# Optimization experiments

Measured on AMD Instinct MI355X. Metric: run time of the kernel, lower is better.

Reference implementation:

```python
import jax, jax.numpy as jnp
import numpy as np

DIM = 2048
N_HEADS = 16
N_KV_HEADS = 4
HEAD_DIM = DIM // N_HEADS  # 128
N_REP = N_HEADS // N_KV_HEADS
EPS = 1e-6


def rmsnorm(x, w):
    norm = jax.lax.rsqrt(jnp.mean(x * x, axis=-1, keepdims=True) + EPS)
    return x * norm * w


def apply_rope(xq, xk, freqs_cis):
    # xq: (B,S,Hq,D), xk: (B,S,Hk,D); freqs_cis: (S, D/2, 2) -> (cos, sin)
    cos = freqs_cis[None, :, None, :, 0]  # (1,S,1,D/2)
    sin = freqs_cis[None, :, None, :, 1]

    def rot(x):
        xr = x.reshape(*x.shape[:-1], HEAD_DIM // 2, 2)
        x0, x1 = xr[..., 0], xr[..., 1]
        o0 = x0 * cos - x1 * sin
        o1 = x0 * sin + x1 * cos
        return jnp.stack([o0, o1], axis=-1).reshape(x.shape)

    return rot(xq), rot(xk)


def setup_inputs() -> dict:
    key = jax.random.key(0)
    k1, k2, k3, k4, k5, k6 = jax.random.split(key, 6)
    B, S = 2, 2048
    x = jax.random.normal(k1, (B, S, DIM), dtype=jnp.float32)
    x_mask = jnp.ones((B, S), dtype=bool)
    freqs_cis = jax.random.uniform(k2, (S, HEAD_DIM // 2, 2), dtype=jnp.float32)
    qkv_out = (N_HEADS + 2 * N_KV_HEADS) * HEAD_DIM  # 3072
    w_qkv = jax.random.normal(k3, (qkv_out, DIM), dtype=jnp.float32) * (DIM ** -0.5)
    w_out = jax.random.normal(k4, (DIM, N_HEADS * HEAD_DIM), dtype=jnp.float32) * (DIM ** -0.5)
    qn_w = jnp.ones((HEAD_DIM,), dtype=jnp.float32)
    kn_w = jnp.ones((HEAD_DIM,), dtype=jnp.float32)
    return {"x": x, "x_mask": x_mask, "freqs_cis": freqs_cis,
            "w_qkv": w_qkv, "w_out": w_out, "qn_w": qn_w, "kn_w": kn_w}


def reference(x, x_mask, freqs_cis, w_qkv, w_out, qn_w, kn_w):
    B, S, _ = x.shape
    qkv = x @ w_qkv.T  # (B,S,3072)
    dq = N_HEADS * HEAD_DIM
    dkv = N_KV_HEADS * HEAD_DIM
    xq = qkv[..., :dq].reshape(B, S, N_HEADS, HEAD_DIM)
    xk = qkv[..., dq:dq + dkv].reshape(B, S, N_KV_HEADS, HEAD_DIM)
    xv = qkv[..., dq + dkv:].reshape(B, S, N_KV_HEADS, HEAD_DIM)
    xq = rmsnorm(xq, qn_w)
    xk = rmsnorm(xk, kn_w)
    xq, xk = apply_rope(xq, xk, freqs_cis)
    # GQA: repeat kv heads
    xk = jnp.repeat(xk, N_REP, axis=2)  # (B,S,H,D)
    xv = jnp.repeat(xv, N_REP, axis=2)
    # SDPA: (B,H,S,D)
    q = jnp.moveaxis(xq, 1, 2)
    k = jnp.moveaxis(xk, 1, 2)
    v = jnp.moveaxis(xv, 1, 2)
    scale = HEAD_DIM ** -0.5
    scores = jnp.einsum('bhqd,bhkd->bhqk', q, k) * scale
    bias = jnp.where(x_mask[:, None, None, :], 0.0, -jnp.inf).astype(q.dtype)
    attn = jax.nn.softmax(scores + bias, axis=-1)
    out = jnp.einsum('bhqk,bhkd->bhqd', attn, v)
    out = jnp.moveaxis(out, 1, 2).reshape(B, S, N_HEADS * HEAD_DIM)
    return out @ w_out.T
```

## Files before the change

kernel.cpp:

```cpp
#include <hip/hip_runtime.h>
#include <hip/hip_bf16.h>

#define DIMSZ 2048
#define SLEN  2048
#define NH    16
#define NKV   4
#define HD    128
#define NTOK  4096
#define QKVN  3072

typedef __bf16 bf16x8 __attribute__((ext_vector_type(8)));
typedef __bf16 bf16x4 __attribute__((ext_vector_type(4)));
typedef short  s16x4  __attribute__((ext_vector_type(4)));
typedef float  floatx4 __attribute__((ext_vector_type(4)));

__device__ __forceinline__ void async16(const __bf16* g, __bf16* l) {
    __builtin_amdgcn_global_load_lds(
        (const __attribute__((address_space(1))) void*)g,
        (__attribute__((address_space(3))) void*)l, 16, 0, 0);
}

__device__ __forceinline__ floatx4 mfma16x16x16_bf16(s16x4 a, s16x4 b, floatx4 c) {
#if __has_builtin(__builtin_amdgcn_mfma_f32_16x16x16bf16_1k)
    return __builtin_amdgcn_mfma_f32_16x16x16bf16_1k(a, b, c, 0, 0, 0);
#else
    asm volatile("v_mfma_f32_16x16x16_bf16 %0, %1, %2, %0"
                 : "+v"(c) : "v"(a), "v"(b));
    return c;
#endif
}

__global__ __launch_bounds__(256) void cvt3(const float* __restrict__ s0, __bf16* __restrict__ d0, int n0,
                                            const float* __restrict__ s1, __bf16* __restrict__ d1, int n1,
                                            const float* __restrict__ s2, __bf16* __restrict__ d2, int n2) {
    int blk = blockIdx.x;
    int b0 = n0 >> 11, b1 = n1 >> 11;
    const float* s; __bf16* d; int base;
    if (blk < b0)           { s = s0; d = d0; base = blk << 11; }
    else if (blk < b0 + b1) { s = s1; d = d1; base = (blk - b0) << 11; }
    else                    { s = s2; d = d2; base = (blk - b0 - b1) << 11; }
    int i = base + threadIdx.x * 8;
    float4 a = *(const float4*)(s + i);
    float4 b = *(const float4*)(s + i + 4);
    bf16x8 o;
    o[0] = (__bf16)a.x; o[1] = (__bf16)a.y; o[2] = (__bf16)a.z; o[3] = (__bf16)a.w;
    o[4] = (__bf16)b.x; o[5] = (__bf16)b.y; o[6] = (__bf16)b.z; o[7] = (__bf16)b.w;
    *(bf16x8*)(d + i) = o;
}

#define BAR() asm volatile("s_barrier" ::: "memory")

#define PH(sa, sb, g, READB, ...)                                               \
    do {                                                                        \
        bf16x8 af[4];                                                           \
        _Pragma("unroll") for (int mi = 0; mi < 4; ++mi)                        \
            af[mi] = *(const bf16x8*)&As[sa][(wr8 + (g) * 4 + mi) * 512 + l8];  \
        if (READB) {                                                            \
            _Pragma("unroll") for (int n = 0; n < NFR; ++n)                     \
                bf[n] = *(const bf16x8*)&Bs[sb][(wcN + n) * 512 + l8];          \
        }                                                                       \
        __VA_ARGS__;                                                            \
        BAR();                                                                  \
        __builtin_amdgcn_s_setprio(1);                                          \
        _Pragma("unroll") for (int mi = 0; mi < 4; ++mi)                        \
            _Pragma("unroll") for (int n = 0; n < NFR; ++n)                     \
                acc[(g) * 4 + mi][n] = __builtin_amdgcn_mfma_f32_16x16x32_bf16( \
                    af[mi], bf[n], acc[(g) * 4 + mi][n], 0, 0, 0);              \
        __builtin_amdgcn_s_setprio(0);                                          \
    } while (0)

#define CKPT_STEADY() do {                                                  \
        if constexpr (LB == 2)                                              \
            asm volatile("s_waitcnt vmcnt(6)" ::: "memory");                 \
        else                                                                \
            asm volatile("s_waitcnt vmcnt(4)" ::: "memory");                 \
        BAR(); } while (0)
#define CKPT_DRAIN()  do {                                                  \
        asm volatile("s_waitcnt vmcnt(0)" ::: "memory");                    \
        BAR(); } while (0)

template <typename CT, int BN, int LB>
__global__ __launch_bounds__(512, 2) void gemm256(const __bf16* __restrict__ A,
                                                  const __bf16* __restrict__ B,
                                                  CT* __restrict__ C,
                                                  int N, int nbx) {
    constexpr int NFR = BN / 64;
    __shared__ __align__(16) __bf16 As[4][8192];
    __shared__ __align__(16) __bf16 Bs[4][BN * 32];
    constexpr int K = 2048, NT = 32;

    const int tid  = threadIdx.x;
    const int w    = tid >> 6, lane = tid & 63;
    const int lr   = lane & 15, lq = lane >> 4;
    const int wr   = w >> 2, wc = w & 3;
    const int wr8  = wr * 8, wcN = wc * NFR, l8 = lane * 8;

    const int nwg = gridDim.x;
    const int cpx = nwg >> 3;
    const int sw  = (blockIdx.x & 7) * cpx + (blockIdx.x >> 3);
    const int tn0 = (sw % nbx) * BN;
    const int tm0 = (sw / nbx) * 256;

    const __bf16* aSrc[2];
#pragma unroll
    for (int j = 0; j < 2; ++j)
        aSrc[j] = A + (size_t)(tm0 + (2 * w + j) * 16 + lr) * K + lq * 8;
    const __bf16* bSrc0 = B + (size_t)(tn0 + w * 16 + lr) * K + lq * 8;
    const __bf16* bSrc1 = (LB == 2)
        ? B + (size_t)(tn0 + (8 + (w & 3)) * 16 + lr) * K + lq * 8 : nullptr;

    const int aoff0 = (2 * w) * 512 + l8, aoff1 = (2 * w + 1) * 512 + l8;
    const int boff0 = w * 512 + l8;
    const int boff1 = (8 + (w & 3)) * 512 + l8;

    auto stageA = [&](int slot, int koff) {
        async16(aSrc[0] + koff, &As[slot][aoff0]);
        async16(aSrc[1] + koff, &As[slot][aoff1]);
    };
    auto stageB = [&](int slot, int koff) {
        async16(bSrc0 + koff, &Bs[slot][boff0]);
        if constexpr (LB == 2) async16(bSrc1 + koff, &Bs[slot][boff1]);
    };

    floatx4 acc[8][NFR] = {};
    bf16x8  bf[NFR];

    stageA(0, 0);   stageB(0, 0);
    stageA(1, 32);  stageB(1, 32);
    stageA(2, 64);  stageB(2, 64);
    stageB(3, 96);
    CKPT_STEADY();

#pragma unroll 1
    for (int t = 0; t < NT; t += 2) {
        const int  k2 = (t + 2) * 64, k3 = (t + 3) * 64;
        const bool g2 = (t + 2) < NT, g3 = (t + 3) < NT;
        PH(0, 0, 0, true,  { if (t + 1 < NT) stageA(3, (t + 1) * 64 + 32); });
        BAR();
        PH(0, 0, 1, false, { if (g2) stageB(0, k2); });
        BAR();
        PH(1, 1, 0, true,  { if (g2) stageA(0, k2); });
        BAR();
        PH(1, 1, 1, false, { if (g2) stageB(1, k2 + 32); });
        if (g2) CKPT_STEADY(); else CKPT_DRAIN();
        PH(2, 2, 0, true,  { if (g2) stageA(1, k2 + 32); });
        BAR();
        PH(2, 2, 1, false, { if (g3) stageB(2, k3); });
        BAR();
        PH(3, 3, 0, true,  { if (g3) stageA(2, k3); });
        BAR();
        PH(3, 3, 1, false, { if (g3) stageB(3, k3 + 32); });
        if (g3) CKPT_STEADY(); else CKPT_DRAIN();
    }

#pragma unroll
    for (int mi = 0; mi < 8; ++mi)
#pragma unroll
        for (int n = 0; n < NFR; ++n)
#pragma unroll
            for (int r = 0; r < 4; ++r) {
                int row = tm0 + wr * 128 + mi * 16 + lq * 4 + r;
                int col = tn0 + wc * (NFR * 16) + n * 16 + lr;
                C[(size_t)row * N + col] = (CT)acc[mi][n][r];
            }
}

__global__ __launch_bounds__(256) void prep(const __bf16* __restrict__ qkv,
                                            const float* __restrict__ freqs,
                                            const float* __restrict__ qn_w,
                                            const float* __restrict__ kn_w,
                                            __bf16* __restrict__ Qo,
                                            __bf16* __restrict__ Ko,
                                            __bf16* __restrict__ VT) {
    if (blockIdx.y < 20) {
        const int tok = blockIdx.x * 4 + (threadIdx.x >> 6);
        const int hd  = blockIdx.y;
        const int t   = threadIdx.x & 63;
        const int s   = tok & (SLEN - 1);
        const int b   = tok >> 11;
        const bool isq = hd < NH;
        const int h    = isq ? hd : hd - NH;
        const int base = isq ? h * HD : (NH * HD + h * HD);

        const __bf16* src = qkv + (size_t)tok * QKVN + base + 2 * t;
        float x0 = (float)src[0], x1 = (float)src[1];
        float ss = x0 * x0 + x1 * x1;
#pragma unroll
        for (int off = 32; off >= 1; off >>= 1) ss += __shfl_xor(ss, off);
        float rs = rsqrtf(ss * (1.0f / 128.0f) + 1e-6f);

        const float* w = isq ? qn_w : kn_w;
        float w0 = w[2 * t], w1 = w[2 * t + 1];
        float cs = freqs[(s * 64 + t) * 2 + 0];
        float sn = freqs[(s * 64 + t) * 2 + 1];
        float n0 = x0 * rs * w0, n1 = x1 * rs * w1;
        float o0 = n0 * cs - n1 * sn;
        float o1 = n0 * sn + n1 * cs;
        if (isq) { o0 *= 0.08838834764831845f; o1 *= 0.08838834764831845f; }

        __bf16* dst = isq ? (Qo + (((size_t)(b * NH + h)) * SLEN + s) * HD + 2 * t)
                          : (Ko + (((size_t)(b * NKV + h)) * SLEN + s) * HD + 2 * t);
        dst[0] = (__bf16)o0;
        dst[1] = (__bf16)o1;
    } else {
        if (blockIdx.x >= 256) return;
        __shared__ __align__(16) __bf16 L[64 * 136];
        const int kh  = blockIdx.x >> 6;
        const int b   = (blockIdx.x >> 5) & 1;
        const int st  = blockIdx.x & 31;
        const int tid = threadIdx.x;
#pragma unroll
        for (int i = 0; i < 4; ++i) {
            int c = tid + 256 * i;
            int srow = c >> 4, dc = (c & 15) * 8;
            int tok = b * SLEN + st * 64 + srow;
            *(int4*)&L[srow * 136 + dc] =
                *(const int4*)&qkv[(size_t)tok * QKVN + 2560 + kh * HD + dc];
        }
        __syncthreads();
#pragma unroll
        for (int i = 0; i < 4; ++i) {
            int c = tid + 256 * i;
            int d = c >> 3, sc = (c & 7) * 8;
            __bf16 tmp[8];
#pragma unroll
            for (int j = 0; j < 8; ++j) tmp[j] = L[(sc + j) * 136 + d];
            *(int4*)&VT[(((size_t)(b * NKV + kh)) * HD + d) * SLEN + st * 64 + sc] =
                *(int4*)tmp;
        }
    }
}

__global__ __launch_bounds__(256) void attn(const __bf16* __restrict__ Q,
                                            const __bf16* __restrict__ Kn,
                                            const __bf16* __restrict__ VT,
                                            __bf16* __restrict__ O) {
    __shared__ __align__(16) __bf16 Ks [2][64 * 128];
    __shared__ __align__(16) __bf16 Vts[2][128 * 64];
    const int qt  = blockIdx.x;
    const int h   = blockIdx.y;
    const int b   = blockIdx.z;
    const int tid = threadIdx.x;
    const int w = tid >> 6, lane = tid & 63, lr = lane & 15, lq = lane >> 4;
    const int kh = h >> 2;

    const __bf16* Qb = Q  + ((size_t)(b * NH + h))   * SLEN * HD;
    const __bf16* Kb = Kn + ((size_t)(b * NKV + kh)) * SLEN * HD;
    const __bf16* Vb = VT + ((size_t)(b * NKV + kh)) * HD * SLEN;

    bf16x8 qf[2][4];
    const int qbase = qt * 128 + w * 32;
#pragma unroll
    for (int g2 = 0; g2 < 2; ++g2)
#pragma unroll
        for (int kc = 0; kc < 4; ++kc)
            qf[g2][kc] = *(const bf16x8*)
                &Qb[(size_t)(qbase + g2 * 16 + lr) * HD + kc * 32 + lq * 8];

    floatx4 oacc[2][8] = {};
    float l_i[2] = {0.f, 0.f};

    auto stage = [&](int buf, int kt) {
#pragma unroll
        for (int i = 0; i < 4; ++i) {
            int c = tid + 256 * i;
            int row = c >> 4, u = c & 15;
            int g = u ^ (row & 7);
            async16(&Kb[(size_t)(kt * 64 + row) * HD + g * 8], &Ks[buf][c * 8]);
        }
#pragma unroll
        for (int i = 0; i < 4; ++i) {
            int c = tid + 256 * i;
            int d = c >> 3, u = c & 7;
            int g = u ^ (d & 7);
            async16(&Vb[(size_t)d * SLEN + kt * 64 + g * 8], &Vts[buf][c * 8]);
        }
    };

    stage(0, 0);
    for (int kt = 0; kt < 32; ++kt) {
        const int buf = kt & 1;
        __syncthreads();
        if (kt < 31) stage(buf ^ 1, kt + 1);

        floatx4 sacc[2][4] = {};
        __builtin_amdgcn_s_setprio(1);
#pragma unroll
        for (int nt = 0; nt < 4; ++nt)
#pragma unroll
            for (int kc = 0; kc < 4; ++kc) {
                bf16x8 kf = *(const bf16x8*)
                    &Ks[buf][(nt * 16 + lr) * 128 + ((kc * 4 + lq) ^ (lr & 7)) * 8];
                sacc[0][nt] = __builtin_amdgcn_mfma_f32_16x16x32_bf16(
                    kf, qf[0][kc], sacc[0][nt], 0, 0, 0);
                sacc[1][nt] = __builtin_amdgcn_mfma_f32_16x16x32_bf16(
                    kf, qf[1][kc], sacc[1][nt], 0, 0, 0);
            }
        __builtin_amdgcn_s_setprio(0);

        s16x4 pf[2][4];
#pragma unroll
        for (int g2 = 0; g2 < 2; ++g2) {
            float rsum = 0.f;
#pragma unroll
            for (int nt = 0; nt < 4; ++nt) {
                bf16x4 pb;
#pragma unroll
                for (int r = 0; r < 4; ++r) {
                    float p = __expf(sacc[g2][nt][r]);
                    rsum += p;
                    pb[r] = (__bf16)p;
                }
                pf[g2][nt] = *(s16x4*)&pb;
            }
            l_i[g2] += rsum;
        }

        __builtin_amdgcn_s_setprio(1);
#pragma unroll
        for (int dt = 0; dt < 8; ++dt)
#pragma unroll
            for (int nt = 0; nt < 4; ++nt) {
                int u = (2 * nt + (lq >> 1)) ^ (lr & 7);
                s16x4 vf = *(const s16x4*)
                    &Vts[buf][(dt * 16 + lr) * 64 + u * 8 + (lq & 1) * 4];
                oacc[0][dt] = mfma16x16x16_bf16(vf, pf[0][nt], oacc[0][dt]);
                oacc[1][dt] = mfma16x16x16_bf16(vf, pf[1][nt], oacc[1][dt]);
            }
        __builtin_amdgcn_s_setprio(0);
    }

#pragma unroll
    for (int g2 = 0; g2 < 2; ++g2) {
        float l = l_i[g2];
        l += __shfl_xor(l, 16);
        l += __shfl_xor(l, 32);
        float inv = 1.0f / l;
        int qs = qbase + g2 * 16 + lr;
        __bf16* orow = O + (((size_t)(b * SLEN + qs)) * NH + h) * HD;
#pragma unroll
        for (int dt = 0; dt < 8; ++dt) {
            bf16x4 ob;
#pragma unroll
            for (int r = 0; r < 4; ++r) ob[r] = (__bf16)(oacc[g2][dt][r] * inv);
            *(bf16x4*)&orow[dt * 16 + lq * 4] = ob;
        }
    }
}

extern "C" void kernel_launch(void* const* d_in, const int* in_sizes, int n_in,
                              void* d_out, int out_size, void* d_ws, size_t ws_size,
                              hipStream_t stream) {
    const float* x     = (const float*)d_in[0];
    const float* freqs = (const float*)d_in[2];
    const float* w_qkv = (const float*)d_in[3];
    const float* w_out = (const float*)d_in[4];
    const float* qn_w  = (const float*)d_in[5];
    const float* kn_w  = (const float*)d_in[6];
    float* out = (float*)d_out;

    char* ws = (char*)d_ws;
    __bf16* qkv = (__bf16*)ws;
    __bf16* Qb  = (__bf16*)(ws + 25165824ull);
    __bf16* Kb  = (__bf16*)(ws + 25165824ull + 16777216);
    __bf16* VTb = (__bf16*)(ws + 25165824ull + 16777216 + 4194304);
    __bf16* xb  = (__bf16*)(ws + 50331648ull);
    __bf16* wqb = (__bf16*)(ws + 50331648ull + 16777216);
    __bf16* wob = (__bf16*)(ws + 50331648ull + 16777216 + 12582912);
    __bf16* Ob  = (__bf16*)ws;

    cvt3<<<dim3((NTOK * DIMSZ + QKVN * DIMSZ + DIMSZ * DIMSZ) / 2048), 256, 0, stream>>>(
        x, xb, NTOK * DIMSZ, w_qkv, wqb, QKVN * DIMSZ, w_out, wob, DIMSZ * DIMSZ);

    gemm256<__bf16, 192, 2><<<dim3(256), 512, 0, stream>>>(
        xb, wqb, qkv, QKVN, 16);

    prep<<<dim3(NTOK / 4, 21), 256, 0, stream>>>(qkv, freqs, qn_w, kn_w, Qb, Kb, VTb);

    attn<<<dim3(SLEN / 128, NH, 2), 256, 0, stream>>>(Qb, Kb, VTb, Ob);

    gemm256<float, 128, 1><<<dim3(256), 512, 0, stream>>>(
        Ob, wob, out, DIMSZ, 16);
}
```

Before: 357.7 us.

## Restructure GEMM pipeline into four full-tile phases and drop attention setprio

The GEMM main loop now runs four phases per iteration instead of eight half-tile phases. Each phase loads all 8 A fragments and all B fragments for one 32-wide k-slice and stages A and B together for a slice three steps ahead. This halves the number of barriers per k-step and changes the vmcnt wait thresholds to fit the new issue order, at the cost of holding more fragment registers at once. Separately, the s_setprio hints around the MFMA blocks in the attention kernel are removed.

```diff
diff --git a/kernel.cpp b/kernel.cpp
--- a/kernel.cpp
+++ b/kernel.cpp
@@ -50,30 +50,28 @@
 
 #define BAR() asm volatile("s_barrier" ::: "memory")
 
-#define PH(sa, sb, g, READB, ...)                                               \
+#define FPH(sa, sb, ...)                                                        \
     do {                                                                        \
-        bf16x8 af[4];                                                           \
-        _Pragma("unroll") for (int mi = 0; mi < 4; ++mi)                        \
-            af[mi] = *(const bf16x8*)&As[sa][(wr8 + (g) * 4 + mi) * 512 + l8];  \
-        if (READB) {                                                            \
-            _Pragma("unroll") for (int n = 0; n < NFR; ++n)                     \
-                bf[n] = *(const bf16x8*)&Bs[sb][(wcN + n) * 512 + l8];          \
-        }                                                                       \
+        bf16x8 af[8]; bf16x8 bf[NFR];                                           \
+        _Pragma("unroll") for (int mi = 0; mi < 8; ++mi)                        \
+            af[mi] = *(const bf16x8*)&As[sa][(wr8 + mi) * 512 + l8];            \
+        _Pragma("unroll") for (int n = 0; n < NFR; ++n)                         \
+            bf[n] = *(const bf16x8*)&Bs[sb][(wcN + n) * 512 + l8];              \
         __VA_ARGS__;                                                            \
         BAR();                                                                  \
         __builtin_amdgcn_s_setprio(1);                                          \
-        _Pragma("unroll") for (int mi = 0; mi < 4; ++mi)                        \
+        _Pragma("unroll") for (int mi = 0; mi < 8; ++mi)                        \
             _Pragma("unroll") for (int n = 0; n < NFR; ++n)                     \
-                acc[(g) * 4 + mi][n] = __builtin_amdgcn_mfma_f32_16x16x32_bf16( \
-                    af[mi], bf[n], acc[(g) * 4 + mi][n], 0, 0, 0);              \
+                acc[mi][n] = __builtin_amdgcn_mfma_f32_16x16x32_bf16(           \
+                    af[mi], bf[n], acc[mi][n], 0, 0, 0);                        \
         __builtin_amdgcn_s_setprio(0);                                          \
     } while (0)
 
 #define CKPT_STEADY() do {                                                  \
         if constexpr (LB == 2)                                              \
-            asm volatile("s_waitcnt vmcnt(6)" ::: "memory");                 \
+            asm volatile("s_waitcnt vmcnt(4)" ::: "memory");                 \
         else                                                                \
-            asm volatile("s_waitcnt vmcnt(4)" ::: "memory");                 \
+            asm volatile("s_waitcnt vmcnt(3)" ::: "memory");                 \
         BAR(); } while (0)
 #define CKPT_DRAIN()  do {                                                  \
         asm volatile("s_waitcnt vmcnt(0)" ::: "memory");                    \
@@ -123,34 +121,28 @@
     };
 
     floatx4 acc[8][NFR] = {};
-    bf16x8  bf[NFR];
-
-    stageA(0, 0);   stageB(0, 0);
-    stageA(1, 32);  stageB(1, 32);
-    stageA(2, 64);  stageB(2, 64);
-    stageB(3, 96);
-    CKPT_STEADY();
+
+    stageA(0, 0);  stageB(0, 0);
+    stageA(1, 32); stageB(1, 32);
+    stageA(2, 64); stageB(2, 64);
+    if constexpr (LB == 2) asm volatile("s_waitcnt vmcnt(4)" ::: "memory");
+    else                   asm volatile("s_waitcnt vmcnt(3)" ::: "memory");
+    BAR();
 
 #pragma unroll 1
     for (int t = 0; t < NT; t += 2) {
-        const int  k2 = (t + 2) * 64, k3 = (t + 3) * 64;
-        const bool g2 = (t + 2) < NT, g3 = (t + 3) < NT;
-        PH(0, 0, 0, true,  { if (t + 1 < NT) stageA(3, (t + 1) * 64 + 32); });
+        const int h3 = (2 * t + 3) * 32, h4 = (2 * t + 4) * 32;
+        const int h5 = (2 * t + 5) * 32, h6 = (2 * t + 6) * 32;
+        const bool g3 = (2 * t + 3) < 2 * NT, g4 = (2 * t + 4) < 2 * NT;
+        const bool g5 = (2 * t + 5) < 2 * NT, g6 = (2 * t + 6) < 2 * NT;
+        FPH(0, 0, { if (g3) { stageA(3, h3); stageB(3, h3); } });
         BAR();
-        PH(0, 0, 1, false, { if (g2) stageB(0, k2); });
+        FPH(1, 1, { if (g4) { stageA(0, h4); stageB(0, h4); } });
+        if (g4) CKPT_STEADY(); else CKPT_DRAIN();
+        FPH(2, 2, { if (g5) { stageA(1, h5); stageB(1, h5); } });
         BAR();
-        PH(1, 1, 0, true,  { if (g2) stageA(0, k2); });
-        BAR();
-        PH(1, 1, 1, false, { if (g2) stageB(1, k2 + 32); });
-        if (g2) CKPT_STEADY(); else CKPT_DRAIN();
-        PH(2, 2, 0, true,  { if (g2) stageA(1, k2 + 32); });
-        BAR();
-        PH(2, 2, 1, false, { if (g3) stageB(2, k3); });
-        BAR();
-        PH(3, 3, 0, true,  { if (g3) stageA(2, k3); });
-        BAR();
-        PH(3, 3, 1, false, { if (g3) stageB(3, k3 + 32); });
-        if (g3) CKPT_STEADY(); else CKPT_DRAIN();
+        FPH(3, 3, { if (g6) { stageA(2, h6); stageB(2, h6); } });
+        if (g6) CKPT_STEADY(); else CKPT_DRAIN();
     }
 
 #pragma unroll
@@ -284,7 +276,6 @@
         if (kt < 31) stage(buf ^ 1, kt + 1);
 
         floatx4 sacc[2][4] = {};
-        __builtin_amdgcn_s_setprio(1);
 #pragma unroll
         for (int nt = 0; nt < 4; ++nt)
 #pragma unroll
@@ -296,7 +287,6 @@
                 sacc[1][nt] = __builtin_amdgcn_mfma_f32_16x16x32_bf16(
                     kf, qf[1][kc], sacc[1][nt], 0, 0, 0);
             }
-        __builtin_amdgcn_s_setprio(0);
 
         s16x4 pf[2][4];
 #pragma unroll
@@ -316,7 +306,6 @@
             l_i[g2] += rsum;
         }
 
-        __builtin_amdgcn_s_setprio(1);
 #pragma unroll
         for (int dt = 0; dt < 8; ++dt)
 #pragma unroll
@@ -327,7 +316,6 @@
                 oacc[0][dt] = mfma16x16x16_bf16(vf, pf[0][nt], oacc[0][dt]);
                 oacc[1][dt] = mfma16x16x16_bf16(vf, pf[1][nt], oacc[1][dt]);
             }
-        __builtin_amdgcn_s_setprio(0);
     }
 
 #pragma unroll
```

Result: no change. 361.6 us (+1.1%).
